# Optimization experiments

Hardware: AMD Instinct MI355X
Metric: run time of the kernel (lower is better)

The kernel has to match this reference:

```python
import jax, jax.numpy as jnp
import numpy as np

H_GRID, W_GRID = 32, 32
MAX_AH, MAX_AW = 3, 3
TOP_K = 64
EPS = 1e-6


def _sum_image(features):
    # features: [B, N, F] with N = H_GRID * W_GRID. Returns area sums [B, A, F]
    # via 2-D integral image, A = sum over (ah,aw) of (H-ah)*(W-aw).
    B, N, F = features.shape
    f2d = features.reshape(B, H_GRID, W_GRID, F)
    integ = jnp.cumsum(jnp.cumsum(f2d, axis=2), axis=1)
    p = jnp.pad(integ, ((0, 0), (1, 0), (1, 0), (0, 0)))  # [B, H+1, W+1, F]
    dst, diag, sh, sv = [], [], [], []
    for ah in range(MAX_AH):
        for aw in range(MAX_AW):
            dst.append(p[:, ah + 1:, aw + 1:, :].reshape(B, -1, F))
            diag.append(p[:, :H_GRID - ah, :W_GRID - aw, :].reshape(B, -1, F))
            sh.append(p[:, ah + 1:, :W_GRID - aw, :].reshape(B, -1, F))
            sv.append(p[:, :H_GRID - ah, aw + 1:, :].reshape(B, -1, F))
    return (jnp.concatenate(dst, 1) - jnp.concatenate(sh, 1)
            - jnp.concatenate(sv, 1) + jnp.concatenate(diag, 1))


def _area_hw():
    # Static per-area heights/widths, shape [A] each.
    hs, ws = [], []
    for ah in range(MAX_AH):
        for aw in range(MAX_AW):
            n = (H_GRID - ah) * (W_GRID - aw)
            hs.append(np.full(n, ah + 1, np.int32))
            ws.append(np.full(n, aw + 1, np.int32))
    return jnp.asarray(np.concatenate(hs)), jnp.asarray(np.concatenate(ws))


def _area_features(x):
    s = _sum_image(x)
    s2 = _sum_image(jnp.square(x))
    heights, widths = _area_hw()
    size = (heights * widths).astype(x.dtype)[None, :, None]
    mean = s / size
    var = s2 / size - jnp.square(mean)
    std = jnp.sqrt(jnp.abs(var) + EPS)
    return mean, std, s, heights, widths


def setup_inputs() -> dict:
    key = jax.random.key(0)
    ks = jax.random.split(key, 9)
    d = 256
    return {
        "q": jax.random.normal(ks[0], (8, 1024, d), jnp.float32),
        "k": jax.random.normal(ks[1], (8, 1024, d), jnp.float32),
        "v": jax.random.normal(ks[2], (8, 1024, d), jnp.float32),
        "emb_h": jax.random.normal(ks[3], (3, d // 2), jnp.float32) * 0.05,
        "emb_w": jax.random.normal(ks[4], (3, d // 2), jnp.float32) * 0.05,
        "W1": jax.random.normal(ks[5], (3 * d, d), jnp.float32) * 0.05,
        "b1": jax.random.normal(ks[6], (d,), jnp.float32) * 0.05,
        "W2": jax.random.normal(ks[7], (d, d), jnp.float32) * 0.05,
        "b2": jax.random.normal(ks[8], (d,), jnp.float32) * 0.05,
    }


def reference(q, k, v, emb_h, emb_w, W1, b1, W2, b2):
    # Area key: mode 'concat' -> MLP(concat(mean, std, size_embed))
    mean, std, _, heights, widths = _area_features(k)
    size_embed = jnp.concatenate([emb_h[heights - 1], emb_w[widths - 1]], axis=-1)  # [A, d]
    B, A = mean.shape[0], mean.shape[1]
    feat = jnp.concatenate(
        [mean, std, jnp.broadcast_to(size_embed[None], (B, A, size_embed.shape[-1]))], axis=-1)
    k_area = jax.nn.relu(feat @ W1 + b1) @ W2 + b2  # [B, A, d]
    # Area value: mode 'sum'
    _, _, v_area, _, _ = _area_features(v)  # [B, A, dv]
    logits = jnp.einsum('bqd,bad->bqa', q, k_area)
    weights = jax.nn.softmax(logits, axis=-1)
    kk = min(TOP_K, weights.shape[-1])
    top_w = jax.lax.top_k(weights, kk)[0]
    min_v = top_w[..., -1:]
    weights = jnp.where(weights >= min_v, weights, jnp.zeros_like(weights))
    weights = weights / jnp.sum(weights, axis=-1, keepdims=True)
    return jnp.einsum('bqa,baf->bqf', weights, v_area)
```

## Files before the change

### kernel.cpp

```cpp
#include <hip/hip_runtime.h>
#include <stdint.h>

#define FD   256
#define NA   8649
#define MT   69192
#define LSTR 8704
#define PB   (33*33*256)

typedef unsigned short ushort_t;
typedef short bf16x8 __attribute__((ext_vector_type(8)));
typedef float f32x4  __attribute__((ext_vector_type(4)));

#define SWZ(r) (((r) >> 2) & 3)

__device__ __forceinline__ unsigned short f2bf(float x) {
  unsigned int u = __float_as_uint(x);
  unsigned int r = (u + 0x7FFFu + ((u >> 16) & 1u)) >> 16;
  return (unsigned short)r;
}
__device__ __forceinline__ float bf2f(unsigned short h) {
  return __uint_as_float(((unsigned int)h) << 16);
}
__device__ __forceinline__ void dec2(float x, unsigned short& h, unsigned short& l) {
  h = f2bf(x);
  l = f2bf(x - bf2f(h));
}

__device__ __forceinline__ void gl2lds(const void* g, void* l) {
  __builtin_amdgcn_global_load_lds(
      (const __attribute__((address_space(1))) void*)g,
      (__attribute__((address_space(3))) void*)l, 16, 0, 0);
}

__device__ __forceinline__ bf16x8 fldq(const ushort_t* plane, int row, int qq) {
  return *(const bf16x8*)(plane + row*32 + ((qq ^ SWZ(row)) << 3));
}

__device__ __forceinline__ f32x4 mfma2(bf16x8 ah, bf16x8 bh, bf16x8 bl, f32x4 acc) {
  acc = __builtin_amdgcn_mfma_f32_16x16x32_bf16(ah, bl, acc, 0, 0, 0);
  acc = __builtin_amdgcn_mfma_f32_16x16x32_bf16(ah, bh, acc, 0, 0, 0);
  return acc;
}
__device__ __forceinline__ f32x4 mfma3(bf16x8 ah, bf16x8 al, bf16x8 bh, bf16x8 bl, f32x4 acc) {
  acc = __builtin_amdgcn_mfma_f32_16x16x32_bf16(al, bh, acc, 0, 0, 0);
  acc = __builtin_amdgcn_mfma_f32_16x16x32_bf16(ah, bl, acc, 0, 0, 0);
  acc = __builtin_amdgcn_mfma_f32_16x16x32_bf16(ah, bh, acc, 0, 0, 0);
  return acc;
}

__global__ __launch_bounds__(256) void k_rowsum(const float* __restrict__ kin,
    const float* __restrict__ vin, float* __restrict__ Pk,
    float* __restrict__ Pk2, float* __restrict__ Pv) {
  int b = blockIdx.x >> 5, i = blockIdx.x & 31;
  int f = threadIdx.x;
  const float* kr = kin + ((size_t)b*1024 + i*32)*FD + f;
  const float* vr = vin + ((size_t)b*1024 + i*32)*FD + f;
  float sk = 0.f, sk2 = 0.f, sv = 0.f;
  size_t base = (size_t)b*PB + (size_t)(i+1)*33*FD + f;
  #pragma unroll
  for (int j = 0; j < 32; ++j) {
    float kv = kr[j*FD], vv = vr[j*FD];
    sk += kv; sk2 += kv*kv; sv += vv;
    size_t p = base + (size_t)(j+1)*FD;
    Pk[p] = sk; Pk2[p] = sk2; Pv[p] = sv;
  }
}

__global__ __launch_bounds__(256) void k_colsum(float* __restrict__ Pk,
    float* __restrict__ Pk2, float* __restrict__ Pv) {
  int j = blockIdx.x, b = blockIdx.y, f = threadIdx.x;
  float* P = (blockIdx.z == 0) ? Pk : (blockIdx.z == 1) ? Pk2 : Pv;
  size_t base = (size_t)b*PB + f;
  if (j == 0) {
    for (int i = 0; i < 33; ++i) P[base + (size_t)i*33*FD] = 0.f;
  } else {
    P[base + (size_t)j*FD] = 0.f;
    float a = 0.f;
    for (int i = 1; i <= 32; ++i) {
      size_t p = base + ((size_t)i*33 + j)*FD;
      a += P[p]; P[p] = a;
    }
  }
}

__global__ __launch_bounds__(256) void k_prep(const float* __restrict__ q,
    const float* __restrict__ W1, const float* __restrict__ W2,
    const float* __restrict__ eh, const float* __restrict__ ew,
    const float* __restrict__ b1,
    ushort_t* __restrict__ qh, ushort_t* __restrict__ ql,
    ushort_t* __restrict__ w1h, ushort_t* __restrict__ w1l,
    ushort_t* __restrict__ w2h, ushort_t* __restrict__ w2l,
    float* __restrict__ bias9, uint32_t* __restrict__ tab) {
  __shared__ float tile[64][65];
  int bx = blockIdx.x, t = threadIdx.x;
  if (bx < 1024) {
    int i = (bx*256 + t) * 8;
    float4 v0 = *(const float4*)(q + i);
    float4 v1 = *(const float4*)(q + i + 4);
    float e[8] = {v0.x, v0.y, v0.z, v0.w, v1.x, v1.y, v1.z, v1.w};
    bf16x8 h8, l8;
    #pragma unroll
    for (int j = 0; j < 8; ++j) {
      unsigned short hu, lu; dec2(e[j], hu, lu);
      h8[j] = (short)hu; l8[j] = (short)lu;
    }
    *(bf16x8*)(qh + i) = h8;
    *(bf16x8*)(ql + i) = l8;
  } else if (bx < 1072) {
    int tb = bx - 1024;
    const float* src; ushort_t* dh; ushort_t* dl; int K, k0, n0;
    if (tb < 32) { src = W1; dh = w1h; dl = w1l; K = 512; k0 = (tb>>2)*64; n0 = (tb&3)*64; }
    else { tb -= 32; src = W2; dh = w2h; dl = w2l; K = 256; k0 = (tb>>2)*64; n0 = (tb&3)*64; }
    int c = t & 63, r4 = t >> 6;
    #pragma unroll
    for (int i = 0; i < 16; ++i) {
      int r = i*4 + r4;
      tile[r][c] = src[(size_t)(k0+r)*FD + n0 + c];
    }
    __syncthreads();
    #pragma unroll
    for (int i = 0; i < 16; ++i) {
      int n = i*4 + r4;
      float x = tile[c][n];
      unsigned short hu, lu; dec2(x, hu, lu);
      dh[(size_t)(n0+n)*K + k0 + c] = hu;
      dl[(size_t)(n0+n)*K + k0 + c] = lu;
    }
  } else if (bx < 1081) {
    int s = bx - 1072, c = t;
    int ah = s/3, aw = s - ah*3;
    float acc = b1[c];
    for (int j = 0; j < 128; ++j) acc += eh[ah*128 + j] * W1[(size_t)(512+j)*FD + c];
    for (int j = 0; j < 128; ++j) acc += ew[aw*128 + j] * W1[(size_t)(640+j)*FD + c];
    bias9[s*FD + c] = acc;
  } else {
    int a = (bx - 1081)*256 + t;
    if (a >= NA) return;
    const int offs[10] = {0,1024,2016,2976,3968,4929,5859,6819,7749,8649};
    int s = 0;
    #pragma unroll
    for (int i = 1; i < 9; ++i) s += (a >= offs[i]) ? 1 : 0;
    int ah = s/3, aw = s - ah*3;
    int idx = a - offs[s];
    int wc = 32 - aw;
    int r = idx / wc;
    int c = idx - r*wc;
    tab[a] = (uint32_t)(r | (c<<6) | (ah<<12) | (aw<<14));
  }
}

__global__ __launch_bounds__(256) void k_xfeat(const float* __restrict__ Pk,
    const float* __restrict__ Pk2, const uint32_t* __restrict__ tab,
    ushort_t* __restrict__ xh) {
  int t = threadIdx.x;
  int row0 = blockIdx.x * 16;
  for (int rr = 0; rr < 16; ++rr) {
    int gr = row0 + rr;
    if (gr >= MT) return;
    int bi = gr / NA;
    int a  = gr - bi*NA;
    uint32_t tb = tab[a];
    int r1 = tb & 63, c1 = (tb>>6)&63, ah=(tb>>12)&3, aw=(tb>>14)&3;
    int r2 = r1+ah+1, c2 = c1+aw+1;
    const float* PKb  = Pk  + (size_t)bi*PB + t;
    const float* PK2b = Pk2 + (size_t)bi*PB + t;
    int i11=(r1*33+c1)*FD, i12=(r1*33+c2)*FD, i21=(r2*33+c1)*FD, i22=(r2*33+c2)*FD;
    float s  = PKb[i22]  - PKb[i12]  - PKb[i21]  + PKb[i11];
    float s2 = PK2b[i22] - PK2b[i12] - PK2b[i21] + PK2b[i11];
    float inv = 1.0f/(float)((ah+1)*(aw+1));
    float mean = s * inv;
    float sd = sqrtf(fabsf(s2*inv - mean*mean) + 1e-6f);
    xh[(size_t)gr*512 + t]       = f2bf(mean);
    xh[(size_t)gr*512 + 256 + t] = f2bf(sd);
  }
}

__global__ __launch_bounds__(512) void k_l1(
    const ushort_t* __restrict__ xh, const ushort_t* __restrict__ w1h,
    const ushort_t* __restrict__ w1l, const float* __restrict__ bias9g,
    const uint32_t* __restrict__ tab, ushort_t* __restrict__ hh) {
  __shared__ __align__(16) char SM[81920];
  ushort_t* SU = (ushort_t*)SM;
  int t = threadIdx.x, lane = t & 63, wid = t >> 6;
  int wr = wid >> 2, wc = wid & 3;
  int row0 = blockIdx.x * 128;

  auto stage = [&](int s, int kc) {
    ushort_t* base = SU + s*20480;
    int r = wid*16 + (lane >> 2);
    int q = lane & 3;
    int rr = row0 + r; if (rr > MT-1) rr = MT-1;
    gl2lds(xh + (size_t)rr*512 + kc + ((q ^ SWZ(r)) << 3), base + wid*512);
    #pragma unroll
    for (int i = 0; i < 2; ++i) {
      int g = 2*wid + i;
      int r2 = g*16 + (lane >> 2);
      int off = (q ^ SWZ(r2)) << 3;
      gl2lds(w1h + (size_t)r2*512 + kc + off, base + 4096  + g*512);
      gl2lds(w1l + (size_t)r2*512 + kc + off, base + 12288 + g*512);
    }
  };

  f32x4 acc[4][4];
  #pragma unroll
  for (int i = 0; i < 4; ++i)
    #pragma unroll
    for (int j = 0; j < 4; ++j) acc[i][j] = (f32x4)0.f;

  stage(0, 0);
  __syncthreads();
  int cur = 0;
  for (int step = 0; step < 16; ++step) {
    if (step < 15) stage(cur ^ 1, (step+1)*32);
    const ushort_t* SA  = SU + cur*20480;
    const ushort_t* SBH = SA + 4096;
    const ushort_t* SBL = SA + 12288;
    int qq = lane >> 4;
    bf16x8 a_[4], bh_[4], bl_[4];
    #pragma unroll
    for (int i = 0; i < 4; ++i) {
      a_[i]  = fldq(SA,  wr*64 + i*16 + (lane & 15), qq);
      bh_[i] = fldq(SBH, wc*64 + i*16 + (lane & 15), qq);
      bl_[i] = fldq(SBL, wc*64 + i*16 + (lane & 15), qq);
    }
    #pragma unroll
    for (int mt = 0; mt < 4; ++mt)
      #pragma unroll
      for (int nt = 0; nt < 4; ++nt)
        acc[mt][nt] = mfma2(a_[mt], bh_[nt], bl_[nt], acc[mt][nt]);
    if (step < 15) { __syncthreads(); cur ^= 1; }
  }

  #pragma unroll
  for (int mt = 0; mt < 4; ++mt) {
    int lrowb = wr*64 + mt*16 + (lane >> 4)*4;
    #pragma unroll
    for (int r = 0; r < 4; ++r) {
      int grow = row0 + lrowb + r;
      if (grow < MT) {
        int a = grow % NA;
        uint32_t tb = tab[a];
        int seg = ((tb>>12)&3)*3 + ((tb>>14)&3);
        const float* bseg = bias9g + seg*FD;
        #pragma unroll
        for (int nt = 0; nt < 4; ++nt) {
          int col = wc*64 + nt*16 + (lane & 15);
          float hv = fmaxf(acc[mt][nt][r] + bseg[col], 0.f);
          hh[(size_t)grow*FD + col] = f2bf(hv);
        }
      }
    }
  }
}

__global__ __launch_bounds__(512) void k_l2(
    const ushort_t* __restrict__ hh, const ushort_t* __restrict__ w2h,
    const ushort_t* __restrict__ w2l, const float* __restrict__ b2,
    ushort_t* __restrict__ kh, ushort_t* __restrict__ kl) {
  __shared__ __align__(16) char SM[81920];
  ushort_t* SU = (ushort_t*)SM;
  int t = threadIdx.x, lane = t & 63, wid = t >> 6;
  int wr = wid >> 2, wc = wid & 3;
  int row0 = blockIdx.x * 128;

  auto stage = [&](int s, int kc) {
    ushort_t* base = SU + s*20480;
    int r = wid*16 + (lane >> 2);
    int q = lane & 3;
    int rr = row0 + r; if (rr > MT-1) rr = MT-1;
    gl2lds(hh + (size_t)rr*FD + kc + ((q ^ SWZ(r)) << 3), base + wid*512);
    #pragma unroll
    for (int i = 0; i < 2; ++i) {
      int g = 2*wid + i;
      int r2 = g*16 + (lane >> 2);
      int off = (q ^ SWZ(r2)) << 3;
      gl2lds(w2h + (size_t)r2*FD + kc + off, base + 4096  + g*512);
      gl2lds(w2l + (size_t)r2*FD + kc + off, base + 12288 + g*512);
    }
  };

  f32x4 acc[4][4];
  #pragma unroll
  for (int i = 0; i < 4; ++i)
    #pragma unroll
    for (int j = 0; j < 4; ++j) acc[i][j] = (f32x4)0.f;

  stage(0, 0);
  __syncthreads();
  int cur = 0;
  for (int step = 0; step < 8; ++step) {
    if (step < 7) stage(cur ^ 1, (step+1)*32);
    const ushort_t* SA  = SU + cur*20480;
    const ushort_t* SBH = SA + 4096;
    const ushort_t* SBL = SA + 12288;
    int qq = lane >> 4;
    bf16x8 a_[4], bh_[4], bl_[4];
    #pragma unroll
    for (int i = 0; i < 4; ++i) {
      a_[i]  = fldq(SA,  wr*64 + i*16 + (lane & 15), qq);
      bh_[i] = fldq(SBH, wc*64 + i*16 + (lane & 15), qq);
      bl_[i] = fldq(SBL, wc*64 + i*16 + (lane & 15), qq);
    }
    #pragma unroll
    for (int mt = 0; mt < 4; ++mt)
      #pragma unroll
      for (int nt = 0; nt < 4; ++nt)
        acc[mt][nt] = mfma2(a_[mt], bh_[nt], bl_[nt], acc[mt][nt]);
    if (step < 7) { __syncthreads(); cur ^= 1; }
  }

  #pragma unroll
  for (int mt = 0; mt < 4; ++mt) {
    int lrowb = wr*64 + mt*16 + (lane >> 4)*4;
    #pragma unroll
    for (int r = 0; r < 4; ++r) {
      int grow = row0 + lrowb + r;
      if (grow < MT) {
        #pragma unroll
        for (int nt = 0; nt < 4; ++nt) {
          int col = wc*64 + nt*16 + (lane & 15);
          float kv = acc[mt][nt][r] + b2[col];
          unsigned short hu, lu; dec2(kv, hu, lu);
          kh[(size_t)grow*FD + col] = hu;
          kl[(size_t)grow*FD + col] = lu;
        }
      }
    }
  }
}

__global__ __launch_bounds__(512, 2) void k_logits(
    const ushort_t* __restrict__ qh, const ushort_t* __restrict__ ql,
    const ushort_t* __restrict__ kh, const ushort_t* __restrict__ kl,
    float* __restrict__ logits, int bbase, int nwg) {
  __shared__ __align__(16) ushort_t SU[2][32768];
  int t = threadIdx.x, lane = t & 63, wid = t >> 6;
  int wr = wid >> 2, wc = wid & 3;
  int bx0 = blockIdx.x;
  int bx = (bx0 & 7) * (nwg >> 3) + (bx0 >> 3);
  int bc = bx / 136;
  int r5 = bx - bc*136;
  int mb = r5 / 34, ab = r5 - mb*34;
  int m0 = mb*256, a0 = ab*256;
  int b = bbase + bc;
  size_t qbase = (size_t)b*1024*FD;
  size_t kbase = (size_t)b*NA*FD;
  float* logW = logits + (size_t)bc*1024*LSTR;

  auto stage = [&](int s, int kc) {
    ushort_t* base = &SU[s][0];
    #pragma unroll
    for (int g2 = 0; g2 < 2; ++g2) {
      int g = wid*2 + g2;
      int ch = g*64 + lane;
      int rr = ch >> 2, sl = ch & 3;
      int off = (sl ^ SWZ(rr)) << 3;
      gl2lds(qh + qbase + (size_t)(m0+rr)*FD + kc + off, base + g*512);
      gl2lds(ql + qbase + (size_t)(m0+rr)*FD + kc + off, base + 8192 + g*512);
      int ar = a0 + rr; if (ar > NA-1) ar = NA-1;
      gl2lds(kh + kbase + (size_t)ar*FD + kc + off, base + 16384 + g*512);
      gl2lds(kl + kbase + (size_t)ar*FD + kc + off, base + 24576 + g*512);
    }
  };

  f32x4 acc[8][4];
  #pragma unroll
  for (int i = 0; i < 8; ++i)
    #pragma unroll
    for (int j = 0; j < 4; ++j) acc[i][j] = (f32x4)0.f;

  stage(0, 0);
  __syncthreads();
  int cur = 0;
  for (int step = 0; step < 8; ++step) {
    if (step < 7) stage(cur ^ 1, (step+1)*32);
    const ushort_t* Ah = &SU[cur][0];
    const ushort_t* Al = Ah + 8192;
    const ushort_t* Bh = Ah + 16384;
    const ushort_t* Bl = Ah + 24576;
    int qq = lane >> 4;
    bf16x8 bhf[4], blf[4];
    #pragma unroll
    for (int nt = 0; nt < 4; ++nt) {
      int rb = wc*64 + nt*16 + (lane & 15);
      bhf[nt] = fldq(Bh, rb, qq);
      blf[nt] = fldq(Bl, rb, qq);
    }
    #pragma unroll
    for (int mt = 0; mt < 8; ++mt) {
      int ra = wr*128 + mt*16 + (lane & 15);
      bf16x8 ahf = fldq(Ah, ra, qq);
      bf16x8 alf = fldq(Al, ra, qq);
      #pragma unroll
      for (int nt = 0; nt < 4; ++nt)
        acc[mt][nt] = mfma3(ahf, alf, bhf[nt], blf[nt], acc[mt][nt]);
    }
    if (step < 7) { __syncthreads(); cur ^= 1; }
  }

  const float NINF = -__builtin_inff();
  #pragma unroll
  for (int mt = 0; mt < 8; ++mt) {
    int m = m0 + wr*128 + mt*16 + (lane >> 4)*4;
    #pragma unroll
    for (int nt = 0; nt < 4; ++nt) {
      int col = a0 + wc*64 + nt*16 + (lane & 15);
      bool ok = (col < NA);
      #pragma unroll
      for (int r = 0; r < 4; ++r)
        logW[(size_t)(m+r)*LSTR + col] = ok ? acc[mt][nt][r] : NINF;
    }
  }
}

__device__ __forceinline__ uint32_t f2key(float x) {
  uint32_t u = __float_as_uint(x);
  return (u & 0x80000000u) ? ~u : (u | 0x80000000u);
}
__device__ __forceinline__ float key2f(uint32_t k) {
  uint32_t u = (k & 0x80000000u) ? (k & 0x7FFFFFFFu) : ~k;
  return __uint_as_float(u);
}

__global__ __launch_bounds__(512) void k_final(const float* __restrict__ logits,
    const float* __restrict__ Pv, const uint32_t* __restrict__ tab,
    float* __restrict__ outp, int bbase) {
  __shared__ int   hist[256];
  __shared__ float redf[8];
  __shared__ int   seli[2];
  __shared__ int   lst[192];
  __shared__ float lw[192];
  __shared__ int4  offs[192];
  __shared__ float accvB[8][256];
  __shared__ int   shcnt;
  __shared__ float cands_v[256];
  __shared__ int   cands_i[256];
  __shared__ int   ncand;
  __shared__ float thrs;
  int t = threadIdx.x;
  int qrow = blockIdx.x & 1023;
  int bc = blockIdx.x >> 10;
  int b = bbase + bc;
  const float* row = logits + ((size_t)bc*1024 + qrow)*LSTR;

  float v[17];
  {
    const float4* row4 = (const float4*)row;
    float4 x0 = row4[t], x1 = row4[t+512], x2 = row4[t+1024], x3 = row4[t+1536];
    v[0]=x0.x; v[1]=x0.y; v[2]=x0.z; v[3]=x0.w;
    v[4]=x1.x; v[5]=x1.y; v[6]=x1.z; v[7]=x1.w;
    v[8]=x2.x; v[9]=x2.y; v[10]=x2.z; v[11]=x2.w;
    v[12]=x3.x; v[13]=x3.y; v[14]=x3.z; v[15]=x3.w;
    v[16]=row[8192 + t];
  }
  float vmax = v[0];
  #pragma unroll
  for (int i = 1; i < 17; ++i) vmax = fmaxf(vmax, v[i]);
  #pragma unroll
  for (int off = 32; off >= 1; off >>= 1) vmax = fmaxf(vmax, __shfl_xor(vmax, off));
  if ((t & 63) == 0) redf[t >> 6] = vmax;
  if (t < 256) hist[t] = 0;
  if (t == 0) { seli[0] = -1; ncand = 0; shcnt = 0; }
  __syncthreads();
  float maxv = fmaxf(fmaxf(fmaxf(redf[0],redf[1]),fmaxf(redf[2],redf[3])),
                     fmaxf(fmaxf(redf[4],redf[5]),fmaxf(redf[6],redf[7])));

  const float SCALE = 8.0f;
  int bins[17];
  #pragma unroll
  for (int i = 0; i < 17; ++i) {
    int bin = (int)((maxv - v[i]) * SCALE);
    bins[i] = bin;
    if ((unsigned)bin < 256u) atomicAdd(&hist[bin], 1);
  }
  __syncthreads();
  if (t < 64) {
    int b0 = t*4;
    int h0 = hist[b0], h1 = hist[b0+1], h2 = hist[b0+2], h3 = hist[b0+3];
    int gsum = h0+h1+h2+h3;
    int pre = gsum;
    #pragma unroll
    for (int d = 1; d < 64; d <<= 1) {
      int o = __shfl_up(pre, d);
      if (t >= d) pre += o;
    }
    pre -= gsum;
    int c0 = pre+h0, c1 = c0+h1, c2 = c1+h2, c3 = c2+h3;
    int cc[4] = {c0, c1, c2, c3};
    int pv[4] = {pre, c0, c1, c2};
    #pragma unroll
    for (int j = 0; j < 4; ++j)
      if (cc[j] >= 64 && pv[j] < 64) { seli[0] = b0 + j; seli[1] = 64 - pv[j]; }
  }
  __syncthreads();
  int tb_bin = seli[0];
  int nc_bin = (tb_bin >= 0) ? hist[tb_bin] : 1000;
  bool fast = (tb_bin >= 0) && (nc_bin <= 256);
  if (fast) {
    int rnk = seli[1];
    #pragma unroll
    for (int i = 0; i < 17; ++i) {
      int idx = (i < 16) ? ((i >> 2)*2048 + 4*t + (i & 3)) : (8192 + t);
      if (bins[i] < tb_bin) {
        int p = atomicAdd(&shcnt, 1);
        if (p < 192) { lst[p] = idx; lw[p] = expf(v[i] - maxv); }
      } else if (bins[i] == tb_bin) {
        int p = atomicAdd(&ncand, 1);
        cands_v[p] = v[i]; cands_i[p] = idx;
      }
    }
    __syncthreads();
    if (t < nc_bin) {
      float ck = cands_v[t];
      int ge = 0, gt = 0;
      for (int j = 0; j < nc_bin; ++j) {
        float cj = cands_v[j];
        ge += (cj >= ck) ? 1 : 0;
        gt += (cj >  ck) ? 1 : 0;
      }
      if (ge >= rnk && gt < rnk) thrs = ck;
    }
    __syncthreads();
    float thrf = thrs;
    for (int j = t; j < nc_bin; j += 512) {
      if (cands_v[j] >= thrf) {
        int p = atomicAdd(&shcnt, 1);
        if (p < 192) { lst[p] = cands_i[j]; lw[p] = expf(cands_v[j] - maxv); }
      }
    }
  } else {
    uint32_t prefix = 0; int need = 64;
    for (int rd = 0; rd < 4; ++rd) {
      int shift = 24 - rd*8;
      uint32_t pmask = (rd == 0) ? 0u : (0xFFFFFFFFu << (shift + 8));
      if (t < 256) hist[t] = 0;
      __syncthreads();
      #pragma unroll
      for (int i = 0; i < 17; ++i) {
        uint32_t ky = f2key(v[i]);
        if ((ky & pmask) == prefix)
          atomicAdd(&hist[(ky >> shift) & 255], 1);
      }
      __syncthreads();
      if (t < 64) {
        int b0 = t*4;
        int h0 = hist[b0], h1 = hist[b0+1], h2 = hist[b0+2], h3 = hist[b0+3];
        int s3 = h3, s2 = h2 + s3, s1 = h1 + s2, s0 = h0 + s1;
        int suf = s0;
        #pragma unroll
        for (int d = 1; d < 64; d <<= 1) {
          int o = __shfl_down(suf, d);
          if (t + d < 64) suf += o;
        }
        int above = suf - s0;
        int cg[5] = { above + s0, above + s1, above + s2, above + s3, above };
        #pragma unroll
        for (int j = 0; j < 4; ++j)
          if (cg[j] >= need && cg[j+1] < need) { seli[0] = b0 + j; seli[1] = need - cg[j+1]; }
      }
      __syncthreads();
      prefix |= ((uint32_t)seli[0]) << shift;
      need = seli[1];
      __syncthreads();
    }
    float thrf = key2f(prefix);
    #pragma unroll
    for (int i = 0; i < 17; ++i) {
      if (v[i] >= thrf) {
        int p = atomicAdd(&shcnt, 1);
        if (p < 192) {
          int idx = (i < 16) ? ((i >> 2)*2048 + 4*t + (i & 3)) : (8192 + t);
          lst[p] = idx;
          lw[p]  = expf(v[i] - maxv);
        }
      }
    }
  }
  __syncthreads();
  int S = min(shcnt, 192);
  if (t < S) {
    int a = lst[t];
    uint32_t tb = tab[a];
    int r1 = tb & 63, c1 = (tb>>6)&63, ah=(tb>>12)&3, aw=(tb>>14)&3;
    int r2 = r1+ah+1, c2 = c1+aw+1;
    offs[t] = make_int4((r1*33+c1)*FD, (r1*33+c2)*FD, (r2*33+c1)*FD, (r2*33+c2)*FD);
  }
  float ssum = 0.f;
  if (t < 64) {
    for (int i = t; i < S; i += 64) ssum += lw[i];
    #pragma unroll
    for (int off = 32; off >= 1; off >>= 1) ssum += __shfl_xor(ssum, off);
    if (t == 0) redf[0] = ssum;
  }
  __syncthreads();
  float inv = 1.0f / redf[0];
  int lf  = (t & 63) << 2;
  int grp = t >> 6;
  const float* Pvb = Pv + (size_t)b*PB + lf;
  float4 a4 = make_float4(0.f, 0.f, 0.f, 0.f);
  auto body = [&](int i) {
    int4 o = offs[i];
    float w = lw[i];
    float4 A = *(const float4*)(Pvb + o.x);
    float4 B = *(const float4*)(Pvb + o.y);
    float4 C = *(const float4*)(Pvb + o.z);
    float4 D = *(const float4*)(Pvb + o.w);
    a4.x += w * (D.x - B.x - C.x + A.x);
    a4.y += w * (D.y - B.y - C.y + A.y);
    a4.z += w * (D.z - B.z - C.z + A.z);
    a4.w += w * (D.w - B.w - C.w + A.w);
  };
  int i = grp;
  for (; i + 8 < S; i += 16) { body(i); body(i + 8); }
  if (i < S) body(i);
  *(float4*)&accvB[grp][lf] = a4;
  __syncthreads();
  if (t < 256) {
    float s = 0.f;
    #pragma unroll
    for (int g = 0; g < 8; ++g) s += accvB[g][t];
    outp[((size_t)b*1024 + qrow)*FD + t] = s * inv;
  }
}

extern "C" void kernel_launch(void* const* d_in, const int* in_sizes, int n_in,
                              void* d_out, int out_size, void* d_ws, size_t ws_size,
                              hipStream_t stream) {
  const float* q  = (const float*)d_in[0];
  const float* k  = (const float*)d_in[1];
  const float* v  = (const float*)d_in[2];
  const float* eh = (const float*)d_in[3];
  const float* ew = (const float*)d_in[4];
  const float* W1 = (const float*)d_in[5];
  const float* b1 = (const float*)d_in[6];
  const float* W2 = (const float*)d_in[7];
  const float* b2 = (const float*)d_in[8];
  float* out = (float*)d_out;

  char* Wp = (char*)d_ws;
  size_t off = 0;
  auto alloc = [&](size_t bytes) -> char* {
    char* p = Wp + off; off += (bytes + 255) & ~(size_t)255; return p;
  };
  const size_t HBYTES = (size_t)MT*FD*2;
  const size_t LBYTES = (size_t)1024*LSTR*4;
  float*    Pv  = (float*)alloc((size_t)8*PB*4);
  ushort_t* qh  = (ushort_t*)alloc((size_t)8*1024*FD*2);
  ushort_t* ql  = (ushort_t*)alloc((size_t)8*1024*FD*2);
  ushort_t* w1h = (ushort_t*)alloc(131072*2);
  ushort_t* w1l = (ushort_t*)alloc(131072*2);
  ushort_t* w2h = (ushort_t*)alloc(65536*2);
  ushort_t* w2l = (ushort_t*)alloc(65536*2);
  float*    bias9 = (float*)alloc(9*FD*4);
  uint32_t* tab = (uint32_t*)alloc(NA*4);
  ushort_t* kh = (ushort_t*)alloc(HBYTES);
  ushort_t* kl = (ushort_t*)alloc(HBYTES);
  size_t offE = off;
  char* E = alloc(2*HBYTES);
  char* F = alloc(HBYTES);
  ushort_t* xh = (ushort_t*)E;
  float* Pk  = (float*)F;
  float* Pk2 = (float*)(F + (size_t)8*PB*4);
  ushort_t* hh = (ushort_t*)F;
  float* logits = (float*)(Wp + offE);

  int c = 1;
  if (ws_size > offE + LBYTES) {
    size_t cap = (ws_size - offE) / LBYTES;
    c = (cap > 8) ? 8 : (int)cap;
    if (c < 1) c = 1;
  }

  k_rowsum<<<dim3(256), dim3(256), 0, stream>>>(k, v, Pk, Pk2, Pv);
  k_colsum<<<dim3(33, 8, 3), dim3(256), 0, stream>>>(Pk, Pk2, Pv);
  k_prep<<<dim3(1115), dim3(256), 0, stream>>>(q, W1, W2, eh, ew, b1,
      qh, ql, w1h, w1l, w2h, w2l, bias9, tab);
  k_xfeat<<<dim3((MT+15)/16), dim3(256), 0, stream>>>(Pk, Pk2, tab, xh);
  k_l1<<<dim3(541), dim3(512), 0, stream>>>(xh, w1h, w1l, bias9, tab, hh);
  k_l2<<<dim3(541), dim3(512), 0, stream>>>(hh, w2h, w2l, b2, kh, kl);
  for (int s0 = 0; s0 < 8; s0 += c) {
    int cc = (8 - s0 < c) ? (8 - s0) : c;
    k_logits<<<dim3(136*cc), dim3(512), 0, stream>>>(qh, ql, kh, kl, logits, s0, 136*cc);
    k_final<<<dim3(1024*cc), dim3(512), 0, stream>>>(logits, Pv, tab, out, s0);
  }
}
```

Measured before the change: 458.8 us.

## Split top-k selection and weighted value gather into separate kernels

The fused final kernel is split in two. A 512-thread selection kernel writes the selected indices, weights and normalizer back into the logits row buffer. A 256-thread gather kernel then reads that compact list and accumulates the integral-image value sums. Each kernel gets its own lighter shared-memory and register footprint, which should raise occupancy for the memory-bound gather phase. The cost is an extra launch and a round trip through global memory for the selected list.

```diff
diff --git a/kernel.cpp b/kernel.cpp
--- a/kernel.cpp
+++ b/kernel.cpp
@@ -422,16 +422,12 @@
   return __uint_as_float(u);
 }
 
-__global__ __launch_bounds__(512) void k_final(const float* __restrict__ logits,
-    const float* __restrict__ Pv, const uint32_t* __restrict__ tab,
-    float* __restrict__ outp, int bbase) {
+__global__ __launch_bounds__(512) void k_select(float* __restrict__ logits, int bbase) {
   __shared__ int   hist[256];
   __shared__ float redf[8];
   __shared__ int   seli[2];
   __shared__ int   lst[192];
   __shared__ float lw[192];
-  __shared__ int4  offs[192];
-  __shared__ float accvB[8][256];
   __shared__ int   shcnt;
   __shared__ float cands_v[256];
   __shared__ int   cands_i[256];
@@ -440,8 +436,7 @@
   int t = threadIdx.x;
   int qrow = blockIdx.x & 1023;
   int bc = blockIdx.x >> 10;
-  int b = bbase + bc;
-  const float* row = logits + ((size_t)bc*1024 + qrow)*LSTR;
+  float* row = logits + ((size_t)bc*1024 + qrow)*LSTR;
 
   float v[17];
   {
@@ -578,29 +573,48 @@
   }
   __syncthreads();
   int S = min(shcnt, 192);
+  float ssum = 0.f;
+  if (t < 64) {
+    for (int i = t; i < S; i += 64) ssum += lw[i];
+    #pragma unroll
+    for (int off = 32; off >= 1; off >>= 1) ssum += __shfl_xor(ssum, off);
+    if (t == 0) redf[0] = ssum;
+  }
+  __syncthreads();
+  float inv = 1.0f / redf[0];
+  if (t == 0) { ((int*)row)[0] = S; row[1] = inv; }
+  if (t < S) ((int2*)(row + 2))[t] = make_int2(lst[t], __float_as_int(lw[t]));
+}
+
+__global__ __launch_bounds__(256) void k_pv(const float* __restrict__ logits,
+    const float* __restrict__ Pv, const uint32_t* __restrict__ tab,
+    float* __restrict__ outp, int bbase) {
+  __shared__ int4  offs[192];
+  __shared__ float lwS[192];
+  __shared__ float accvB[4][256];
+  int t = threadIdx.x;
+  int qrow = blockIdx.x & 1023;
+  int bc = blockIdx.x >> 10;
+  int b = bbase + bc;
+  const float* row = logits + ((size_t)bc*1024 + qrow)*LSTR;
+  int S = ((const int*)row)[0];
+  float inv = row[1];
   if (t < S) {
-    int a = lst[t];
-    uint32_t tb = tab[a];
+    int2 e = ((const int2*)(row + 2))[t];
+    uint32_t tb = tab[e.x];
     int r1 = tb & 63, c1 = (tb>>6)&63, ah=(tb>>12)&3, aw=(tb>>14)&3;
     int r2 = r1+ah+1, c2 = c1+aw+1;
     offs[t] = make_int4((r1*33+c1)*FD, (r1*33+c2)*FD, (r2*33+c1)*FD, (r2*33+c2)*FD);
-  }
-  float ssum = 0.f;
-  if (t < 64) {
-    for (int i = t; i < S; i += 64) ssum += lw[i];
-    #pragma unroll
-    for (int off = 32; off >= 1; off >>= 1) ssum += __shfl_xor(ssum, off);
-    if (t == 0) redf[0] = ssum;
-  }
-  __syncthreads();
-  float inv = 1.0f / redf[0];
+    lwS[t]  = __int_as_float(e.y);
+  }
+  __syncthreads();
   int lf  = (t & 63) << 2;
   int grp = t >> 6;
   const float* Pvb = Pv + (size_t)b*PB + lf;
   float4 a4 = make_float4(0.f, 0.f, 0.f, 0.f);
   auto body = [&](int i) {
     int4 o = offs[i];
-    float w = lw[i];
+    float w = lwS[i];
     float4 A = *(const float4*)(Pvb + o.x);
     float4 B = *(const float4*)(Pvb + o.y);
     float4 C = *(const float4*)(Pvb + o.z);
@@ -611,14 +625,12 @@
     a4.w += w * (D.w - B.w - C.w + A.w);
   };
   int i = grp;
-  for (; i + 8 < S; i += 16) { body(i); body(i + 8); }
+  for (; i + 4 < S; i += 8) { body(i); body(i + 4); }
   if (i < S) body(i);
   *(float4*)&accvB[grp][lf] = a4;
   __syncthreads();
-  if (t < 256) {
-    float s = 0.f;
-    #pragma unroll
-    for (int g = 0; g < 8; ++g) s += accvB[g][t];
+  {
+    float s = accvB[0][t] + accvB[1][t] + accvB[2][t] + accvB[3][t];
     outp[((size_t)b*1024 + qrow)*FD + t] = s * inv;
   }
 }
@@ -681,6 +693,7 @@
   for (int s0 = 0; s0 < 8; s0 += c) {
     int cc = (8 - s0 < c) ? (8 - s0) : c;
     k_logits<<<dim3(136*cc), dim3(512), 0, stream>>>(qh, ql, kh, kl, logits, s0, 136*cc);
-    k_final<<<dim3(1024*cc), dim3(512), 0, stream>>>(logits, Pv, tab, out, s0);
-  }
-}
+    k_select<<<dim3(1024*cc), dim3(512), 0, stream>>>(logits, s0);
+    k_pv<<<dim3(1024*cc), dim3(256), 0, stream>>>(logits, Pv, tab, out, s0);
+  }
+}
```

Result: slower. 475.2 us (+3.6%).
